# Kernel optimization log

Measured on AMD Instinct MI355X. Metric: run time of the kernel, lower is better.

The kernel has to match this reference:

```python
import jax, jax.numpy as jnp
import numpy as np

INF = 1e10
EPS = 1e-5
B, S, H, NH = 4, 1024, 1024, 16


def _linear(x, W, b):
    return x @ W + b


def _layernorm(x, g, b):
    mean = x.mean(-1, keepdims=True)
    var = ((x - mean) ** 2).mean(-1, keepdims=True)  # biased, matches .pow(2).mean
    return g * (x - mean) / jnp.sqrt(var + EPS) + b


def _mha(xq, xkv, mask, Wq, bq, Wk, bk, Wv, bv, Wo, bo, num_head):
    Bq, Sq, Hd = xq.shape
    d = Hd // num_head
    scale = jnp.asarray(np.sqrt(d), xq.dtype)
    q = _linear(xq, Wq, bq).reshape(Bq, Sq, num_head, d).transpose(0, 2, 1, 3)
    k = _linear(xkv, Wk, bk).reshape(Bq, -1, num_head, d).transpose(0, 2, 1, 3)
    v = _linear(xkv, Wv, bv).reshape(Bq, -1, num_head, d).transpose(0, 2, 1, 3)
    scores = jnp.einsum('bhqd,bhkd->bhqk', q, k) / scale
    # mask [B,Skv] -> additive; NOTE: original divides (scores+mask) by scale AGAIN
    add = (1.0 - mask[:, None, None, :].astype(scores.dtype)) * (-INF)
    att = jax.nn.softmax((scores + add) / scale, axis=-1)
    out = jnp.einsum('bhqk,bhkd->bhqd', att, v).transpose(0, 2, 1, 3).reshape(Bq, Sq, Hd)
    return _linear(out, Wo, bo)


def _block(hidden_states, self_att_mask, cross_hidden_states, cross_att_mask,
           sWq, sbq, sWk, sbk, sWv, sbv, sWo, sbo,
           cWq, cbq, cWk, cbk, cWv, cbv, cWo, cbo,
           g, b, W1, b1, W2, b2, num_head):
    sa = _mha(hidden_states, hidden_states, self_att_mask,
              sWq, sbq, sWk, sbk, sWv, sbv, sWo, sbo, num_head)
    sa_n = _layernorm(sa + hidden_states, g, b)
    ca = _mha(sa_n, cross_hidden_states, cross_att_mask,
              cWq, cbq, cWk, cbk, cWv, cbv, cWo, cbo, num_head)
    # NOTE: residual uses the ORIGINAL hidden_states, matching the source
    h = _layernorm(ca + hidden_states, g, b)
    ff = _linear(jax.nn.relu(_linear(h, W1, b1)), W2, b2)
    return _layernorm(ff + h, g, b)


def setup_inputs() -> dict:
    key = jax.random.key(0)
    ks = jax.random.split(key, 20)
    std = 0.02
    def lin(k, din, dout):
        k1, k2 = jax.random.split(k)
        return (jax.random.normal(k1, (din, dout), jnp.float32) * std,
                jax.random.normal(k2, (dout,), jnp.float32) * std)
    inp = {
        'hidden_states': jax.random.normal(ks[0], (B, S, H), jnp.float32),
        'self_att_mask': jnp.ones((B, S), jnp.int32),
        'cross_hidden_states': jax.random.normal(ks[1], (B, S, H), jnp.float32),
        'cross_att_mask': jnp.ones((B, S), jnp.int32),
        'num_head': NH,
    }
    names = ['sWq sbq', 'sWk sbk', 'sWv sbv', 'sWo sbo',
             'cWq cbq', 'cWk cbk', 'cWv cbv', 'cWo cbo']
    for i, nm in enumerate(names):
        wn, bn = nm.split()
        W, bb = lin(ks[2 + i], H, H)
        inp[wn] = W
        inp[bn] = bb
    inp['g'] = jnp.ones((H,), jnp.float32)
    inp['b'] = jnp.zeros((H,), jnp.float32)
    inp['W1'], inp['b1'] = lin(ks[12], H, 4 * H)
    inp['W2'], inp['b2'] = lin(ks[13], 4 * H, H)
    return inp


def reference(hidden_states, self_att_mask, cross_hidden_states, cross_att_mask,
              num_head, sWq, sbq, sWk, sbk, sWv, sbv, sWo, sbo,
              cWq, cbq, cWk, cbk, cWv, cbv, cWo, cbo,
              g, b, W1, b1, W2, b2):
    return _block(hidden_states, self_att_mask, cross_hidden_states, cross_att_mask,
                  sWq, sbq, sWk, sbk, sWv, sbv, sWo, sbo,
                  cWq, cbq, cWk, cbk, cWv, cbv, cWo, cbo,
                  g, b, W1, b1, W2, b2, num_head)
```

## Files before the change

kernel.cpp:

```cpp
#include <hip/hip_runtime.h>
#include <hip/hip_bf16.h>


typedef float float4v __attribute__((ext_vector_type(4)));
typedef __bf16 bf16x8 __attribute__((ext_vector_type(8)));
typedef unsigned short ushort8 __attribute__((ext_vector_type(8)));
typedef unsigned int uint2v __attribute__((ext_vector_type(2)));

__device__ __forceinline__ unsigned short f2bf1(float f) {
    unsigned u = __builtin_bit_cast(unsigned, f);
    u += 0x7fffu + ((u >> 16) & 1u);
    return (unsigned short)(u >> 16);
}
__device__ __forceinline__ unsigned f2bf2(float lo, float hi) {
    unsigned a = __builtin_bit_cast(unsigned, lo);
    a += 0x7fffu + ((a >> 16) & 1u);
    unsigned b = __builtin_bit_cast(unsigned, hi);
    b += 0x7fffu + ((b >> 16) & 1u);
    return (a >> 16) | (b & 0xffff0000u);
}
__device__ __forceinline__ bf16x8 ldsv8(const unsigned short* p) {
    return __builtin_bit_cast(bf16x8, *(const ushort8*)p);
}
__device__ __forceinline__ void async16(const unsigned short* g, unsigned short* l) {
    __builtin_amdgcn_global_load_lds(
        (const __attribute__((address_space(1))) unsigned int*)(g),
        (__attribute__((address_space(3))) unsigned int*)(l),
        16, 0, 0);
}

template <int RELU, int OUT_BF16, int DBUF, int ORDER>
__global__ __launch_bounds__(256) void gemm_bt(
    const unsigned short* __restrict__ A, const unsigned short* __restrict__ Bt,
    const float* __restrict__ bias, void* __restrict__ Cout,
    int M, int N, int K)
{
    __shared__ __align__(16) unsigned short As[(DBUF ? 2 : 1) * 128 * 64];
    __shared__ __align__(16) unsigned short Bs[(DBUF ? 2 : 1) * 128 * 64];

    const int tid = threadIdx.x;
    const int m0 = (ORDER ? blockIdx.x : blockIdx.y) * 128;
    const int n0 = (ORDER ? blockIdx.y : blockIdx.x) * 128;
    const int w = tid >> 6, lane = tid & 63;
    const int lr = lane & 15, quad = lane >> 4;
    const int wm = (w >> 1) * 64, wn = (w & 1) * 64;

    const int sr = lane >> 3, sc = lane & 7;
    const int fch = sc ^ sr;
    const unsigned short* Ag = A + (size_t)(m0 + w * 32 + sr) * K + fch * 8;
    const unsigned short* Bg = Bt + (size_t)(n0 + w * 32 + sr) * K + fch * 8;

    float4v acc[4][4];
#pragma unroll
    for (int i = 0; i < 4; i++)
#pragma unroll
        for (int j = 0; j < 4; j++) acc[i][j] = 0.f;

    const int ch0 = quad ^ (lr & 7);
    const int ch1 = (4 + quad) ^ (lr & 7);

    auto issue = [&](int buf, int k0) {
        unsigned short* Al = &As[buf * (128 * 64) + (w * 32) * 64];
        unsigned short* Bl = &Bs[buf * (128 * 64) + (w * 32) * 64];
#pragma unroll
        for (int i = 0; i < 4; i++) {
            async16(Ag + (size_t)(i * 8) * K + k0, Al + (i * 8) * 64);
            async16(Bg + (size_t)(i * 8) * K + k0, Bl + (i * 8) * 64);
        }
    };
    auto compute = [&](int buf) {
        const unsigned short* Ab = &As[buf * (128 * 64)];
        const unsigned short* Bb = &Bs[buf * (128 * 64)];
#pragma unroll
        for (int kk = 0; kk < 2; kk++) {
            const int ch = kk ? ch1 : ch0;
            bf16x8 af[4], bf[4];
#pragma unroll
            for (int i = 0; i < 4; i++) {
                af[i] = ldsv8(&Ab[(wm + i * 16 + lr) * 64 + ch * 8]);
                bf[i] = ldsv8(&Bb[(wn + i * 16 + lr) * 64 + ch * 8]);
            }
#pragma unroll
            for (int i = 0; i < 4; i++)
#pragma unroll
                for (int j = 0; j < 4; j++)
                    acc[i][j] = __builtin_amdgcn_mfma_f32_16x16x32_bf16(af[i], bf[j], acc[i][j], 0, 0, 0);
        }
    };

    if (DBUF) {
        const int NIT = K >> 6;
        issue(0, 0);
        for (int it = 0; it < NIT; ++it) {
            const int nxt = it + 1;
            if (nxt < NIT) {
                issue(nxt & 1, nxt << 6);
                __builtin_amdgcn_sched_barrier(0);
                __builtin_amdgcn_s_waitcnt(0x0F78);
            } else {
                __builtin_amdgcn_sched_barrier(0);
                __builtin_amdgcn_s_waitcnt(0x0F70);
            }
            __builtin_amdgcn_s_barrier();
            __builtin_amdgcn_sched_barrier(0);
            compute(it & 1);
            __builtin_amdgcn_sched_barrier(0);
            __builtin_amdgcn_s_barrier();
            __builtin_amdgcn_sched_barrier(0);
        }
    } else {
        for (int k0 = 0; k0 < K; k0 += 64) {
            issue(0, k0);
            __syncthreads();
            compute(0);
            __syncthreads();
        }
    }

#pragma unroll
    for (int j = 0; j < 4; j++) {
        const int col = n0 + wn + j * 16 + lr;
        const float bv = bias[col];
#pragma unroll
        for (int i = 0; i < 4; i++) {
            const int row0 = m0 + wm + i * 16 + quad * 4;
#pragma unroll
            for (int r = 0; r < 4; r++) {
                float v = acc[i][j][r] + bv;
                if (RELU) v = fmaxf(v, 0.f);
                if (OUT_BF16)
                    ((unsigned short*)Cout)[(size_t)(row0 + r) * N + col] = f2bf1(v);
                else
                    ((float*)Cout)[(size_t)(row0 + r) * N + col] = v;
            }
        }
    }
}

__global__ __launch_bounds__(256) void attn_mfma(
    const unsigned short* __restrict__ Q, int qs,
    const unsigned short* __restrict__ K, const unsigned short* __restrict__ V, int kvs,
    const int* __restrict__ mask, unsigned short* __restrict__ O)
{
    __shared__ __align__(16) unsigned short Ks[64 * 64];
    __shared__ __align__(16) unsigned short Vt[64][72];
    __shared__ __align__(16) unsigned short Pb[128][72];
    __shared__ float madd[64];

    const int tid = threadIdx.x;
    const int b = blockIdx.z, h = blockIdx.y, q0 = blockIdx.x * 128;
    const int w = tid >> 6, lane = tid & 63;
    const int lr = lane & 15, quad = lane >> 4;
    const int wm = w * 32;
    const float4v zf = {0.f, 0.f, 0.f, 0.f};

    bf16x8 qf[2][2];
#pragma unroll
    for (int i = 0; i < 2; i++)
#pragma unroll
        for (int c = 0; c < 2; c++)
            qf[i][c] = ldsv8(Q + (size_t)(b * 1024 + q0 + wm + i * 16 + lr) * qs
                             + h * 64 + c * 32 + quad * 8);

    const int sr = lane >> 3, sc = lane & 7;
    const int fch = sc ^ sr;
    const int ch0 = quad ^ (lr & 7), ch1 = (4 + quad) ^ (lr & 7);
    const int vkey = tid & 63, vseg = (tid >> 6) * 16;

    float4v oac[2][4];
    float m_reg[2][4], l_reg[2][4];
#pragma unroll
    for (int i = 0; i < 2; i++) {
#pragma unroll
        for (int j = 0; j < 4; j++) oac[i][j] = zf;
#pragma unroll
        for (int rr = 0; rr < 4; rr++) { m_reg[i][rr] = -3e38f; l_reg[i][rr] = 0.f; }
    }

    for (int kb = 0; kb < 16; ++kb) {
        const int s0 = kb * 64;
        __syncthreads();
#pragma unroll
        for (int i = 0; i < 2; i++)
            async16(K + (size_t)(b * 1024 + s0 + w * 16 + i * 8 + sr) * kvs + h * 64 + fch * 8,
                    &Ks[(w * 16 + i * 8) * 64]);
        {
            const unsigned short* vp = V + (size_t)(b * 1024 + s0 + vkey) * kvs + h * 64 + vseg;
            ushort8 v0 = *(const ushort8*)vp;
            ushort8 v1 = *(const ushort8*)(vp + 8);
#pragma unroll
            for (int j = 0; j < 8; j++) {
                Vt[vseg + j][vkey] = v0[j];
                Vt[vseg + 8 + j][vkey] = v1[j];
            }
        }
        if (tid < 64)
            madd[tid] = (1.0f - (float)mask[b * 1024 + s0 + tid]) * (-1.25e9f);
        __syncthreads();

        float4v sa[2][4];
#pragma unroll
        for (int j = 0; j < 4; j++) {
            const int krow = j * 16 + lr;
            bf16x8 kf0 = ldsv8(&Ks[krow * 64 + ch0 * 8]);
            bf16x8 kf1 = ldsv8(&Ks[krow * 64 + ch1 * 8]);
            sa[0][j] = __builtin_amdgcn_mfma_f32_16x16x32_bf16(qf[0][0], kf0, zf, 0, 0, 0);
            sa[0][j] = __builtin_amdgcn_mfma_f32_16x16x32_bf16(qf[0][1], kf1, sa[0][j], 0, 0, 0);
            sa[1][j] = __builtin_amdgcn_mfma_f32_16x16x32_bf16(qf[1][0], kf0, zf, 0, 0, 0);
            sa[1][j] = __builtin_amdgcn_mfma_f32_16x16x32_bf16(qf[1][1], kf1, sa[1][j], 0, 0, 0);
        }
#pragma unroll
        for (int j = 0; j < 4; j++) {
            const float ma = madd[j * 16 + lr];
            sa[0][j] = sa[0][j] * 0.015625f + ma;
            sa[1][j] = sa[1][j] * 0.015625f + ma;
        }

#pragma unroll
        for (int i = 0; i < 2; i++) {
#pragma unroll
            for (int rr = 0; rr < 4; rr++) {
                float rm = fmaxf(fmaxf(sa[i][0][rr], sa[i][1][rr]),
                                 fmaxf(sa[i][2][rr], sa[i][3][rr]));
                rm = fmaxf(rm, __shfl_xor(rm, 1));
                rm = fmaxf(rm, __shfl_xor(rm, 2));
                rm = fmaxf(rm, __shfl_xor(rm, 4));
                rm = fmaxf(rm, __shfl_xor(rm, 8));
                float mnew = fmaxf(m_reg[i][rr], rm);
                float al = __expf(m_reg[i][rr] - mnew);
                float p0 = __expf(sa[i][0][rr] - mnew);
                float p1 = __expf(sa[i][1][rr] - mnew);
                float p2 = __expf(sa[i][2][rr] - mnew);
                float p3 = __expf(sa[i][3][rr] - mnew);
                float rs = p0 + p1 + p2 + p3;
                rs += __shfl_xor(rs, 1);
                rs += __shfl_xor(rs, 2);
                rs += __shfl_xor(rs, 4);
                rs += __shfl_xor(rs, 8);
                l_reg[i][rr] = l_reg[i][rr] * al + rs;
                m_reg[i][rr] = mnew;
                const int row = wm + i * 16 + quad * 4 + rr;
                Pb[row][ 0 + lr] = f2bf1(p0);
                Pb[row][16 + lr] = f2bf1(p1);
                Pb[row][32 + lr] = f2bf1(p2);
                Pb[row][48 + lr] = f2bf1(p3);
                oac[i][0][rr] *= al;
                oac[i][1][rr] *= al;
                oac[i][2][rr] *= al;
                oac[i][3][rr] *= al;
            }
        }

        bf16x8 pf[2][2];
#pragma unroll
        for (int i = 0; i < 2; i++)
#pragma unroll
            for (int c = 0; c < 2; c++)
                pf[i][c] = ldsv8(&Pb[wm + i * 16 + lr][c * 32 + quad * 8]);
#pragma unroll
        for (int j = 0; j < 4; j++) {
            bf16x8 vf0 = ldsv8(&Vt[j * 16 + lr][quad * 8]);
            bf16x8 vf1 = ldsv8(&Vt[j * 16 + lr][32 + quad * 8]);
            oac[0][j] = __builtin_amdgcn_mfma_f32_16x16x32_bf16(pf[0][0], vf0, oac[0][j], 0, 0, 0);
            oac[0][j] = __builtin_amdgcn_mfma_f32_16x16x32_bf16(pf[0][1], vf1, oac[0][j], 0, 0, 0);
            oac[1][j] = __builtin_amdgcn_mfma_f32_16x16x32_bf16(pf[1][0], vf0, oac[1][j], 0, 0, 0);
            oac[1][j] = __builtin_amdgcn_mfma_f32_16x16x32_bf16(pf[1][1], vf1, oac[1][j], 0, 0, 0);
        }
    }

#pragma unroll
    for (int i = 0; i < 2; i++)
#pragma unroll
        for (int rr = 0; rr < 4; rr++) {
            const float inv = 1.0f / l_reg[i][rr];
            const int row = q0 + wm + i * 16 + quad * 4 + rr;
            unsigned short* op = O + (size_t)(b * 1024 + row) * 1024 + h * 64;
#pragma unroll
            for (int j = 0; j < 4; j++)
                op[j * 16 + lr] = f2bf1(oac[i][j][rr] * inv);
        }
}

__global__ __launch_bounds__(256) void add_ln_kernel(
    const float* __restrict__ X, const float* __restrict__ R,
    const float* __restrict__ g, const float* __restrict__ bb,
    float* __restrict__ outF, unsigned short* __restrict__ outB)
{
    const int row = blockIdx.x, tid = threadIdx.x;
    const float4v* x4 = (const float4v*)(X + (size_t)row * 1024);
    const float4v* r4 = (const float4v*)(R + (size_t)row * 1024);
    float4v z = x4[tid] + r4[tid];
    float s = z.x + z.y + z.z + z.w;
    float sq = z.x * z.x + z.y * z.y + z.z * z.z + z.w * z.w;
#pragma unroll
    for (int off = 32; off > 0; off >>= 1) {
        s += __shfl_down(s, off);
        sq += __shfl_down(sq, off);
    }
    __shared__ float ws[4], wsq[4];
    __shared__ float sm, sr;
    if ((tid & 63) == 0) { ws[tid >> 6] = s; wsq[tid >> 6] = sq; }
    __syncthreads();
    if (tid == 0) {
        float S1 = ws[0] + ws[1] + ws[2] + ws[3];
        float S2 = wsq[0] + wsq[1] + wsq[2] + wsq[3];
        float mean = S1 * (1.0f / 1024.0f);
        float var = S2 * (1.0f / 1024.0f) - mean * mean;
        sm = mean;
        sr = rsqrtf(var + 1e-5f);
    }
    __syncthreads();
    const float mean = sm, rstd = sr;
    const float4v* g4 = (const float4v*)g;
    const float4v* b4 = (const float4v*)bb;
    float4v res = g4[tid] * ((z - mean) * rstd) + b4[tid];
    if (outF) ((float4v*)(outF + (size_t)row * 1024))[tid] = res;
    if (outB) {
        uint2v u = { f2bf2(res.x, res.y), f2bf2(res.z, res.w) };
        *(uint2v*)(outB + (size_t)row * 1024 + tid * 4) = u;
    }
}

__device__ __forceinline__ void tconv_body(const float* __restrict__ S,
                                           unsigned short* __restrict__ D,
                                           int R, int C, int r0, int c0)
{
    __shared__ float tile[64][65];
    const int tid = threadIdx.x;
    const int tr = tid >> 4, tc4 = (tid & 15) * 4;
#pragma unroll
    for (int i = 0; i < 4; i++) {
        const int rr = i * 16 + tr;
        *(float4v*)&tile[rr][tc4] = *(const float4v*)(S + (size_t)(r0 + rr) * C + c0 + tc4);
    }
    __syncthreads();
#pragma unroll
    for (int i = 0; i < 4; i++) {
        const int dr = i * 16 + tr;
        float v0 = tile[tc4 + 0][dr];
        float v1 = tile[tc4 + 1][dr];
        float v2 = tile[tc4 + 2][dr];
        float v3 = tile[tc4 + 3][dr];
        uint2v u = { f2bf2(v0, v1), f2bf2(v2, v3) };
        *(uint2v*)(D + (size_t)(c0 + dr) * R + r0 + tc4) = u;
    }
}
__global__ __launch_bounds__(256) void transpose_conv(
    const float* __restrict__ S, unsigned short* __restrict__ D, int R, int C)
{
    tconv_body(S, D, R, C, blockIdx.y * 64, blockIdx.x * 64);
}
__global__ __launch_bounds__(256) void transpose8(
    const float* s0, const float* s1, const float* s2, const float* s3,
    const float* s4, const float* s5, const float* s6, const float* s7,
    unsigned short* d0, unsigned short* d1, unsigned short* d2, unsigned short* d3,
    unsigned short* d4, unsigned short* d5, unsigned short* d6, unsigned short* d7)
{
    const float* S;
    unsigned short* D;
    switch (blockIdx.z) {
        case 0: S = s0; D = d0; break;
        case 1: S = s1; D = d1; break;
        case 2: S = s2; D = d2; break;
        case 3: S = s3; D = d3; break;
        case 4: S = s4; D = d4; break;
        case 5: S = s5; D = d5; break;
        case 6: S = s6; D = d6; break;
        default: S = s7; D = d7; break;
    }
    tconv_body(S, D, 1024, 1024, blockIdx.y * 64, blockIdx.x * 64);
}

__global__ __launch_bounds__(256) void convert_bf16(
    const float* __restrict__ s0, unsigned short* __restrict__ d0,
    const float* __restrict__ s1, unsigned short* __restrict__ d1)
{
    const float* s = blockIdx.y ? s1 : s0;
    unsigned short* d = blockIdx.y ? d1 : d0;
    const size_t i = ((size_t)blockIdx.x * 256 + threadIdx.x) * 4;
    float4v v = *(const float4v*)(s + i);
    uint2v u = { f2bf2(v.x, v.y), f2bf2(v.z, v.w) };
    *(uint2v*)(d + i) = u;
}

__global__ __launch_bounds__(256) void biascat(
    const float* __restrict__ sbq, const float* __restrict__ sbk, const float* __restrict__ sbv,
    const float* __restrict__ cbk, const float* __restrict__ cbv,
    float* __restrict__ bq, float* __restrict__ bc)
{
    const int i = blockIdx.x * 256 + threadIdx.x;
    if (i < 3072)
        bq[i] = i < 1024 ? sbq[i] : (i < 2048 ? sbk[i - 1024] : sbv[i - 2048]);
    else {
        const int j = i - 3072;
        bc[j] = j < 1024 ? cbk[j] : cbv[j - 1024];
    }
}

extern "C" void kernel_launch(void* const* d_in, const int* in_sizes, int n_in,
                              void* d_out, int out_size, void* d_ws, size_t ws_size,
                              hipStream_t stream)
{
    const float* x     = (const float*)d_in[0];
    const int*   smask = (const int*)d_in[1];
    const float* cx    = (const float*)d_in[2];
    const int*   cmask = (const int*)d_in[3];
    const float* sWq = (const float*)d_in[5],  *sbq = (const float*)d_in[6];
    const float* sWk = (const float*)d_in[7],  *sbk = (const float*)d_in[8];
    const float* sWv = (const float*)d_in[9],  *sbv = (const float*)d_in[10];
    const float* sWo = (const float*)d_in[11], *sbo = (const float*)d_in[12];
    const float* cWq = (const float*)d_in[13], *cbq = (const float*)d_in[14];
    const float* cWk = (const float*)d_in[15], *cbk = (const float*)d_in[16];
    const float* cWv = (const float*)d_in[17], *cbv = (const float*)d_in[18];
    const float* cWo = (const float*)d_in[19], *cbo = (const float*)d_in[20];
    const float* g   = (const float*)d_in[21], *bb  = (const float*)d_in[22];
    const float* W1  = (const float*)d_in[23], *b1  = (const float*)d_in[24];
    const float* W2  = (const float*)d_in[25], *b2  = (const float*)d_in[26];
    float* out = (float*)d_out;

    const size_t MB = 1024 * 1024;
    unsigned char* ws = (unsigned char*)d_ws;
    unsigned short* xb   = (unsigned short*)(ws + 0 * MB);
    unsigned short* cxb  = (unsigned short*)(ws + 8 * MB);
    unsigned short* SANb = (unsigned short*)(ws + 16 * MB);
    unsigned short* QKV  = (unsigned short*)(ws + 24 * MB);
    unsigned short* CQ   = (unsigned short*)(ws + 24 * MB);
    unsigned short* CKV  = (unsigned short*)(ws + 32 * MB);
    unsigned short* T    = (unsigned short*)(ws + 48 * MB);
    float*          Af   = (float*)(ws + 56 * MB);
    float*          HH   = (float*)(ws + 72 * MB);
    unsigned short* HHb  = (unsigned short*)(ws + 88 * MB);
    unsigned short* WtQKV = (unsigned short*)(ws + 96 * MB);
    unsigned short* WtCKV = (unsigned short*)(ws + 102 * MB);
    unsigned short* WtSWO = (unsigned short*)(ws + 106 * MB);
    unsigned short* WtCWQ = (unsigned short*)(ws + 108 * MB);
    unsigned short* WtCWO = (unsigned short*)(ws + 110 * MB);
    unsigned short* WtW1  = (unsigned short*)(ws + 112 * MB);
    unsigned short* WtW2  = (unsigned short*)(ws + 120 * MB);
    float* biasQ = (float*)(ws + 128 * MB);
    float* biasC = (float*)(ws + 128 * MB + 16 * 1024);
    unsigned short* MID = (unsigned short*)(ws + 0 * MB);

    dim3 blk(256);

    convert_bf16<<<dim3(4096, 2), blk, 0, stream>>>(x, xb, cx, cxb);
    transpose8<<<dim3(16, 16, 8), blk, 0, stream>>>(
        sWq, sWk, sWv, cWk, cWv, sWo, cWq, cWo,
        WtQKV, WtQKV + 1024 * 1024, WtQKV + 2 * 1024 * 1024,
        WtCKV, WtCKV + 1024 * 1024,
        WtSWO, WtCWQ, WtCWO);
    transpose_conv<<<dim3(64, 16), blk, 0, stream>>>(W1, WtW1, 1024, 4096);
    transpose_conv<<<dim3(16, 64), blk, 0, stream>>>(W2, WtW2, 4096, 1024);
    biascat<<<20, blk, 0, stream>>>(sbq, sbk, sbv, cbk, cbv, biasQ, biasC);

    gemm_bt<0, 1, 0, 1><<<dim3(32, 24), blk, 0, stream>>>(xb, WtQKV, biasQ, QKV, 4096, 3072, 1024);
    attn_mfma<<<dim3(8, 16, 4), blk, 0, stream>>>(QKV, 3072, QKV + 1024, QKV + 2048, 3072, smask, T);
    gemm_bt<0, 0, 1, 1><<<dim3(32, 8), blk, 0, stream>>>(T, WtSWO, sbo, Af, 4096, 1024, 1024);
    add_ln_kernel<<<4096, blk, 0, stream>>>(Af, x, g, bb, nullptr, SANb);

    gemm_bt<0, 1, 1, 1><<<dim3(32, 8), blk, 0, stream>>>(SANb, WtCWQ, cbq, CQ, 4096, 1024, 1024);
    gemm_bt<0, 1, 1, 1><<<dim3(32, 16), blk, 0, stream>>>(cxb, WtCKV, biasC, CKV, 4096, 2048, 1024);
    attn_mfma<<<dim3(8, 16, 4), blk, 0, stream>>>(CQ, 1024, CKV, CKV + 1024, 2048, cmask, T);
    gemm_bt<0, 0, 1, 1><<<dim3(32, 8), blk, 0, stream>>>(T, WtCWO, cbo, Af, 4096, 1024, 1024);
    add_ln_kernel<<<4096, blk, 0, stream>>>(Af, x, g, bb, HH, HHb);

    gemm_bt<1, 1, 0, 0><<<dim3(32, 32), blk, 0, stream>>>(HHb, WtW1, b1, MID, 4096, 4096, 1024);
    gemm_bt<0, 0, 1, 1><<<dim3(32, 8), blk, 0, stream>>>(MID, WtW2, b2, Af, 4096, 1024, 4096);
    add_ln_kernel<<<4096, blk, 0, stream>>>(Af, HH, g, bb, out, nullptr);
}
```

Before: 582.3 us.

## Split-K the N=1024 GEMMs and shrink attention tiles with swizzled LDS

```diff
diff --git a/kernel.cpp b/kernel.cpp
--- a/kernel.cpp
+++ b/kernel.cpp
@@ -41,14 +41,16 @@
     const int tid = threadIdx.x;
     const int m0 = (ORDER ? blockIdx.x : blockIdx.y) * 128;
     const int n0 = (ORDER ? blockIdx.y : blockIdx.x) * 128;
+    const int KL = K / gridDim.z;
+    const int kbase = blockIdx.z * KL;
     const int w = tid >> 6, lane = tid & 63;
     const int lr = lane & 15, quad = lane >> 4;
     const int wm = (w >> 1) * 64, wn = (w & 1) * 64;
 
     const int sr = lane >> 3, sc = lane & 7;
     const int fch = sc ^ sr;
-    const unsigned short* Ag = A + (size_t)(m0 + w * 32 + sr) * K + fch * 8;
-    const unsigned short* Bg = Bt + (size_t)(n0 + w * 32 + sr) * K + fch * 8;
+    const unsigned short* Ag = A + (size_t)(m0 + w * 32 + sr) * K + kbase + fch * 8;
+    const unsigned short* Bg = Bt + (size_t)(n0 + w * 32 + sr) * K + kbase + fch * 8;
 
     float4v acc[4][4];
 #pragma unroll
@@ -89,7 +91,7 @@
     };
 
     if (DBUF) {
-        const int NIT = K >> 6;
+        const int NIT = KL >> 6;
         issue(0, 0);
         for (int it = 0; it < NIT; ++it) {
             const int nxt = it + 1;
@@ -109,7 +111,7 @@
             __builtin_amdgcn_sched_barrier(0);
         }
     } else {
-        for (int k0 = 0; k0 < K; k0 += 64) {
+        for (int k0 = 0; k0 < KL; k0 += 64) {
             issue(0, k0);
             __syncthreads();
             compute(0);
@@ -120,7 +122,7 @@
 #pragma unroll
     for (int j = 0; j < 4; j++) {
         const int col = n0 + wn + j * 16 + lr;
-        const float bv = bias[col];
+        const float bv = bias ? bias[col] : 0.f;
 #pragma unroll
         for (int i = 0; i < 4; i++) {
             const int row0 = m0 + wm + i * 16 + quad * 4;
@@ -131,7 +133,7 @@
                 if (OUT_BF16)
                     ((unsigned short*)Cout)[(size_t)(row0 + r) * N + col] = f2bf1(v);
                 else
-                    ((float*)Cout)[(size_t)(row0 + r) * N + col] = v;
+                    ((float*)Cout)[(size_t)blockIdx.z * M * N + (size_t)(row0 + r) * N + col] = v;
             }
         }
     }
@@ -143,39 +145,38 @@
     const int* __restrict__ mask, unsigned short* __restrict__ O)
 {
     __shared__ __align__(16) unsigned short Ks[64 * 64];
-    __shared__ __align__(16) unsigned short Vt[64][72];
-    __shared__ __align__(16) unsigned short Pb[128][72];
+    __shared__ __align__(16) unsigned short Vt[64 * 64];
+    __shared__ __align__(16) unsigned short Pb[64 * 64];
     __shared__ float madd[64];
 
     const int tid = threadIdx.x;
-    const int b = blockIdx.z, h = blockIdx.y, q0 = blockIdx.x * 128;
+    const int b = blockIdx.z, h = blockIdx.y, q0 = blockIdx.x * 64;
     const int w = tid >> 6, lane = tid & 63;
     const int lr = lane & 15, quad = lane >> 4;
-    const int wm = w * 32;
     const float4v zf = {0.f, 0.f, 0.f, 0.f};
 
-    bf16x8 qf[2][2];
-#pragma unroll
-    for (int i = 0; i < 2; i++)
-#pragma unroll
-        for (int c = 0; c < 2; c++)
-            qf[i][c] = ldsv8(Q + (size_t)(b * 1024 + q0 + wm + i * 16 + lr) * qs
-                             + h * 64 + c * 32 + quad * 8);
+    bf16x8 qf[2];
+#pragma unroll
+    for (int c = 0; c < 2; c++)
+        qf[c] = ldsv8(Q + (size_t)(b * 1024 + q0 + w * 16 + lr) * qs
+                      + h * 64 + c * 32 + quad * 8);
 
     const int sr = lane >> 3, sc = lane & 7;
     const int fch = sc ^ sr;
     const int ch0 = quad ^ (lr & 7), ch1 = (4 + quad) ^ (lr & 7);
-    const int vkey = tid & 63, vseg = (tid >> 6) * 16;
-
-    float4v oac[2][4];
-    float m_reg[2][4], l_reg[2][4];
-#pragma unroll
-    for (int i = 0; i < 2; i++) {
-#pragma unroll
-        for (int j = 0; j < 4; j++) oac[i][j] = zf;
-#pragma unroll
-        for (int rr = 0; rr < 4; rr++) { m_reg[i][rr] = -3e38f; l_reg[i][rr] = 0.f; }
-    }
+
+    const int vk = tid & 15, vh = tid >> 7;
+    const int vkb = vk + vh * 32;
+    const int vseg = ((tid >> 4) & 7) * 8;
+    const int pospair = vk * 4 + vh * 2;
+    const int vchunk = pospair >> 3, voff = pospair & 7;
+
+    float4v oac[4];
+    float m_reg[4], l_reg[4];
+#pragma unroll
+    for (int j = 0; j < 4; j++) oac[j] = zf;
+#pragma unroll
+    for (int rr = 0; rr < 4; rr++) { m_reg[rr] = -3e38f; l_reg[rr] = 0.f; }
 
     for (int kb = 0; kb < 16; ++kb) {
         const int s0 = kb * 64;
@@ -185,111 +186,98 @@
             async16(K + (size_t)(b * 1024 + s0 + w * 16 + i * 8 + sr) * kvs + h * 64 + fch * 8,
                     &Ks[(w * 16 + i * 8) * 64]);
         {
-            const unsigned short* vp = V + (size_t)(b * 1024 + s0 + vkey) * kvs + h * 64 + vseg;
+            const unsigned short* vp = V + (size_t)(b * 1024 + s0 + vkb) * kvs + h * 64 + vseg;
             ushort8 v0 = *(const ushort8*)vp;
-            ushort8 v1 = *(const ushort8*)(vp + 8);
+            ushort8 v1 = *(const ushort8*)(vp + (size_t)16 * kvs);
 #pragma unroll
             for (int j = 0; j < 8; j++) {
-                Vt[vseg + j][vkey] = v0[j];
-                Vt[vseg + 8 + j][vkey] = v1[j];
+                const int row = vseg + j;
+                const int schv = vchunk ^ (row & 7);
+                *(unsigned*)&Vt[row * 64 + schv * 8 + voff] =
+                    (unsigned)v0[j] | ((unsigned)v1[j] << 16);
             }
         }
         if (tid < 64)
             madd[tid] = (1.0f - (float)mask[b * 1024 + s0 + tid]) * (-1.25e9f);
         __syncthreads();
 
-        float4v sa[2][4];
+        float4v sa[4];
 #pragma unroll
         for (int j = 0; j < 4; j++) {
             const int krow = j * 16 + lr;
             bf16x8 kf0 = ldsv8(&Ks[krow * 64 + ch0 * 8]);
             bf16x8 kf1 = ldsv8(&Ks[krow * 64 + ch1 * 8]);
-            sa[0][j] = __builtin_amdgcn_mfma_f32_16x16x32_bf16(qf[0][0], kf0, zf, 0, 0, 0);
-            sa[0][j] = __builtin_amdgcn_mfma_f32_16x16x32_bf16(qf[0][1], kf1, sa[0][j], 0, 0, 0);
-            sa[1][j] = __builtin_amdgcn_mfma_f32_16x16x32_bf16(qf[1][0], kf0, zf, 0, 0, 0);
-            sa[1][j] = __builtin_amdgcn_mfma_f32_16x16x32_bf16(qf[1][1], kf1, sa[1][j], 0, 0, 0);
-        }
+            sa[j] = __builtin_amdgcn_mfma_f32_16x16x32_bf16(qf[0], kf0, zf, 0, 0, 0);
+            sa[j] = __builtin_amdgcn_mfma_f32_16x16x32_bf16(qf[1], kf1, sa[j], 0, 0, 0);
+        }
+#pragma unroll
+        for (int j = 0; j < 4; j++)
+            sa[j] = sa[j] * 0.015625f + madd[j * 16 + lr];
+
+#pragma unroll
+        for (int rr = 0; rr < 4; rr++) {
+            float rm = fmaxf(fmaxf(sa[0][rr], sa[1][rr]), fmaxf(sa[2][rr], sa[3][rr]));
+            rm = fmaxf(rm, __shfl_xor(rm, 1));
+            rm = fmaxf(rm, __shfl_xor(rm, 2));
+            rm = fmaxf(rm, __shfl_xor(rm, 4));
+            rm = fmaxf(rm, __shfl_xor(rm, 8));
+            const float mnew = fmaxf(m_reg[rr], rm);
+            const float al = __expf(m_reg[rr] - mnew);
+            const float p0 = __expf(sa[0][rr] - mnew);
+            const float p1 = __expf(sa[1][rr] - mnew);
+            const float p2 = __expf(sa[2][rr] - mnew);
+            const float p3 = __expf(sa[3][rr] - mnew);
+            float rs = p0 + p1 + p2 + p3;
+            rs += __shfl_xor(rs, 1);
+            rs += __shfl_xor(rs, 2);
+            rs += __shfl_xor(rs, 4);
+            rs += __shfl_xor(rs, 8);
+            l_reg[rr] = l_reg[rr] * al + rs;
+            m_reg[rr] = mnew;
+            const int row = w * 16 + quad * 4 + rr;
+            const int schp = (lr >> 1) ^ (row & 7);
+            uint2v pk = { f2bf2(p0, p1), f2bf2(p2, p3) };
+            *(uint2v*)&Pb[row * 64 + schp * 8 + (lr & 1) * 4] = pk;
+            oac[0][rr] *= al;
+            oac[1][rr] *= al;
+            oac[2][rr] *= al;
+            oac[3][rr] *= al;
+        }
+
+        bf16x8 pf0 = ldsv8(&Pb[(w * 16 + lr) * 64 + ch0 * 8]);
+        bf16x8 pf1 = ldsv8(&Pb[(w * 16 + lr) * 64 + ch1 * 8]);
 #pragma unroll
         for (int j = 0; j < 4; j++) {
-            const float ma = madd[j * 16 + lr];
-            sa[0][j] = sa[0][j] * 0.015625f + ma;
-            sa[1][j] = sa[1][j] * 0.015625f + ma;
-        }
-
-#pragma unroll
-        for (int i = 0; i < 2; i++) {
-#pragma unroll
-            for (int rr = 0; rr < 4; rr++) {
-                float rm = fmaxf(fmaxf(sa[i][0][rr], sa[i][1][rr]),
-                                 fmaxf(sa[i][2][rr], sa[i][3][rr]));
-                rm = fmaxf(rm, __shfl_xor(rm, 1));
-                rm = fmaxf(rm, __shfl_xor(rm, 2));
-                rm = fmaxf(rm, __shfl_xor(rm, 4));
-                rm = fmaxf(rm, __shfl_xor(rm, 8));
-                float mnew = fmaxf(m_reg[i][rr], rm);
-                float al = __expf(m_reg[i][rr] - mnew);
-                float p0 = __expf(sa[i][0][rr] - mnew);
-                float p1 = __expf(sa[i][1][rr] - mnew);
-                float p2 = __expf(sa[i][2][rr] - mnew);
-                float p3 = __expf(sa[i][3][rr] - mnew);
-                float rs = p0 + p1 + p2 + p3;
-                rs += __shfl_xor(rs, 1);
-                rs += __shfl_xor(rs, 2);
-                rs += __shfl_xor(rs, 4);
-                rs += __shfl_xor(rs, 8);
-                l_reg[i][rr] = l_reg[i][rr] * al + rs;
-                m_reg[i][rr] = mnew;
-                const int row = wm + i * 16 + quad * 4 + rr;
-                Pb[row][ 0 + lr] = f2bf1(p0);
-                Pb[row][16 + lr] = f2bf1(p1);
-                Pb[row][32 + lr] = f2bf1(p2);
-                Pb[row][48 + lr] = f2bf1(p3);
-                oac[i][0][rr] *= al;
-                oac[i][1][rr] *= al;
-                oac[i][2][rr] *= al;
-                oac[i][3][rr] *= al;
-            }
-        }
-
-        bf16x8 pf[2][2];
-#pragma unroll
-        for (int i = 0; i < 2; i++)
-#pragma unroll
-            for (int c = 0; c < 2; c++)
-                pf[i][c] = ldsv8(&Pb[wm + i * 16 + lr][c * 32 + quad * 8]);
-#pragma unroll
-        for (int j = 0; j < 4; j++) {
-            bf16x8 vf0 = ldsv8(&Vt[j * 16 + lr][quad * 8]);
-            bf16x8 vf1 = ldsv8(&Vt[j * 16 + lr][32 + quad * 8]);
-            oac[0][j] = __builtin_amdgcn_mfma_f32_16x16x32_bf16(pf[0][0], vf0, oac[0][j], 0, 0, 0);
-            oac[0][j] = __builtin_amdgcn_mfma_f32_16x16x32_bf16(pf[0][1], vf1, oac[0][j], 0, 0, 0);
-            oac[1][j] = __builtin_amdgcn_mfma_f32_16x16x32_bf16(pf[1][0], vf0, oac[1][j], 0, 0, 0);
-            oac[1][j] = __builtin_amdgcn_mfma_f32_16x16x32_bf16(pf[1][1], vf1, oac[1][j], 0, 0, 0);
-        }
-    }
-
-#pragma unroll
-    for (int i = 0; i < 2; i++)
-#pragma unroll
-        for (int rr = 0; rr < 4; rr++) {
-            const float inv = 1.0f / l_reg[i][rr];
-            const int row = q0 + wm + i * 16 + quad * 4 + rr;
-            unsigned short* op = O + (size_t)(b * 1024 + row) * 1024 + h * 64;
-#pragma unroll
-            for (int j = 0; j < 4; j++)
-                op[j * 16 + lr] = f2bf1(oac[i][j][rr] * inv);
-        }
-}
-
+            bf16x8 vf0 = ldsv8(&Vt[(j * 16 + lr) * 64 + ch0 * 8]);
+            bf16x8 vf1 = ldsv8(&Vt[(j * 16 + lr) * 64 + ch1 * 8]);
+            oac[j] = __builtin_amdgcn_mfma_f32_16x16x32_bf16(pf0, vf0, oac[j], 0, 0, 0);
+            oac[j] = __builtin_amdgcn_mfma_f32_16x16x32_bf16(pf1, vf1, oac[j], 0, 0, 0);
+        }
+    }
+
+#pragma unroll
+    for (int rr = 0; rr < 4; rr++) {
+        const float inv = 1.0f / l_reg[rr];
+        const int row = q0 + w * 16 + quad * 4 + rr;
+        unsigned short* op = O + (size_t)(b * 1024 + row) * 1024 + h * 64;
+#pragma unroll
+        for (int j = 0; j < 4; j++)
+            op[j * 16 + lr] = f2bf1(oac[j][rr] * inv);
+    }
+}
+
+#define PSTRIDE ((size_t)4096 * 1024)
 __global__ __launch_bounds__(256) void add_ln_kernel(
-    const float* __restrict__ X, const float* __restrict__ R,
+    const float* __restrict__ P, int nparts, const float* __restrict__ lbias,
+    const float* __restrict__ R,
     const float* __restrict__ g, const float* __restrict__ bb,
     float* __restrict__ outF, unsigned short* __restrict__ outB)
 {
     const int row = blockIdx.x, tid = threadIdx.x;
-    const float4v* x4 = (const float4v*)(X + (size_t)row * 1024);
-    const float4v* r4 = (const float4v*)(R + (size_t)row * 1024);
-    float4v z = x4[tid] + r4[tid];
+    float4v z = ((const float4v*)(R + (size_t)row * 1024))[tid];
+    for (int p = 0; p < nparts; ++p)
+        z += ((const float4v*)(P + p * PSTRIDE + (size_t)row * 1024))[tid];
+    if (lbias) z += ((const float4v*)lbias)[tid];
     float s = z.x + z.y + z.z + z.w;
     float sq = z.x * z.x + z.y * z.y + z.z * z.z + z.w * z.w;
 #pragma unroll
@@ -423,23 +411,23 @@
     unsigned short* xb   = (unsigned short*)(ws + 0 * MB);
     unsigned short* cxb  = (unsigned short*)(ws + 8 * MB);
     unsigned short* SANb = (unsigned short*)(ws + 16 * MB);
-    unsigned short* QKV  = (unsigned short*)(ws + 24 * MB);
     unsigned short* CQ   = (unsigned short*)(ws + 24 * MB);
+    unsigned short* MID  = (unsigned short*)(ws + 0 * MB);
+    unsigned short* QKV  = (unsigned short*)(ws + 32 * MB);
     unsigned short* CKV  = (unsigned short*)(ws + 32 * MB);
-    unsigned short* T    = (unsigned short*)(ws + 48 * MB);
-    float*          Af   = (float*)(ws + 56 * MB);
-    float*          HH   = (float*)(ws + 72 * MB);
-    unsigned short* HHb  = (unsigned short*)(ws + 88 * MB);
-    unsigned short* WtQKV = (unsigned short*)(ws + 96 * MB);
-    unsigned short* WtCKV = (unsigned short*)(ws + 102 * MB);
-    unsigned short* WtSWO = (unsigned short*)(ws + 106 * MB);
-    unsigned short* WtCWQ = (unsigned short*)(ws + 108 * MB);
-    unsigned short* WtCWO = (unsigned short*)(ws + 110 * MB);
-    unsigned short* WtW1  = (unsigned short*)(ws + 112 * MB);
-    unsigned short* WtW2  = (unsigned short*)(ws + 120 * MB);
-    float* biasQ = (float*)(ws + 128 * MB);
-    float* biasC = (float*)(ws + 128 * MB + 16 * 1024);
-    unsigned short* MID = (unsigned short*)(ws + 0 * MB);
+    unsigned short* T    = (unsigned short*)(ws + 56 * MB);
+    float*          P    = (float*)(ws + 64 * MB);
+    float*          HH   = (float*)(ws + 96 * MB);
+    unsigned short* HHb  = (unsigned short*)(ws + 112 * MB);
+    unsigned short* WtQKV = (unsigned short*)(ws + 120 * MB);
+    unsigned short* WtCKV = (unsigned short*)(ws + 126 * MB);
+    unsigned short* WtSWO = (unsigned short*)(ws + 130 * MB);
+    unsigned short* WtCWQ = (unsigned short*)(ws + 132 * MB);
+    unsigned short* WtCWO = (unsigned short*)(ws + 134 * MB);
+    unsigned short* WtW1  = (unsigned short*)(ws + 136 * MB);
+    unsigned short* WtW2  = (unsigned short*)(ws + 144 * MB);
+    float* biasQ = (float*)(ws + 152 * MB);
+    float* biasC = (float*)(ws + 152 * MB + 16 * 1024);
 
     dim3 blk(256);
 
@@ -454,17 +442,17 @@
     biascat<<<20, blk, 0, stream>>>(sbq, sbk, sbv, cbk, cbv, biasQ, biasC);
 
     gemm_bt<0, 1, 0, 1><<<dim3(32, 24), blk, 0, stream>>>(xb, WtQKV, biasQ, QKV, 4096, 3072, 1024);
-    attn_mfma<<<dim3(8, 16, 4), blk, 0, stream>>>(QKV, 3072, QKV + 1024, QKV + 2048, 3072, smask, T);
-    gemm_bt<0, 0, 1, 1><<<dim3(32, 8), blk, 0, stream>>>(T, WtSWO, sbo, Af, 4096, 1024, 1024);
-    add_ln_kernel<<<4096, blk, 0, stream>>>(Af, x, g, bb, nullptr, SANb);
+    attn_mfma<<<dim3(16, 16, 4), blk, 0, stream>>>(QKV, 3072, QKV + 1024, QKV + 2048, 3072, smask, T);
+    gemm_bt<0, 0, 1, 1><<<dim3(32, 8, 2), blk, 0, stream>>>(T, WtSWO, nullptr, P, 4096, 1024, 1024);
+    add_ln_kernel<<<4096, blk, 0, stream>>>(P, 2, sbo, x, g, bb, nullptr, SANb);
 
     gemm_bt<0, 1, 1, 1><<<dim3(32, 8), blk, 0, stream>>>(SANb, WtCWQ, cbq, CQ, 4096, 1024, 1024);
     gemm_bt<0, 1, 1, 1><<<dim3(32, 16), blk, 0, stream>>>(cxb, WtCKV, biasC, CKV, 4096, 2048, 1024);
-    attn_mfma<<<dim3(8, 16, 4), blk, 0, stream>>>(CQ, 1024, CKV, CKV + 1024, 2048, cmask, T);
-    gemm_bt<0, 0, 1, 1><<<dim3(32, 8), blk, 0, stream>>>(T, WtCWO, cbo, Af, 4096, 1024, 1024);
-    add_ln_kernel<<<4096, blk, 0, stream>>>(Af, x, g, bb, HH, HHb);
+    attn_mfma<<<dim3(16, 16, 4), blk, 0, stream>>>(CQ, 1024, CKV, CKV + 1024, 2048, cmask, T);
+    gemm_bt<0, 0, 1, 1><<<dim3(32, 8, 2), blk, 0, stream>>>(T, WtCWO, nullptr, P, 4096, 1024, 1024);
+    add_ln_kernel<<<4096, blk, 0, stream>>>(P, 2, cbo, x, g, bb, HH, HHb);
 
     gemm_bt<1, 1, 0, 0><<<dim3(32, 32), blk, 0, stream>>>(HHb, WtW1, b1, MID, 4096, 4096, 1024);
-    gemm_bt<0, 0, 1, 1><<<dim3(32, 8), blk, 0, stream>>>(MID, WtW2, b2, Af, 4096, 1024, 4096);
-    add_ln_kernel<<<4096, blk, 0, stream>>>(Af, HH, g, bb, out, nullptr);
-}
+    gemm_bt<0, 0, 1, 1><<<dim3(32, 8, 2), blk, 0, stream>>>(MID, WtW2, nullptr, P, 4096, 1024, 4096);
+    add_ln_kernel<<<4096, blk, 0, stream>>>(P, 2, b2, HH, g, bb, out, nullptr);
+}
```

Measured after the change: 528.5 us. 9.2% less time.

## Split-K output GEMMs, pre-transpose V in epilogue, drop online softmax max

Applied to the files above, without the earlier changes.

```diff
diff --git a/kernel.cpp b/kernel.cpp
--- a/kernel.cpp
+++ b/kernel.cpp
@@ -6,6 +6,8 @@
 typedef __bf16 bf16x8 __attribute__((ext_vector_type(8)));
 typedef unsigned short ushort8 __attribute__((ext_vector_type(8)));
 typedef unsigned int uint2v __attribute__((ext_vector_type(2)));
+
+#define VBIG (1 << 29)
 
 __device__ __forceinline__ unsigned short f2bf1(float f) {
     unsigned u = __builtin_bit_cast(unsigned, f);
@@ -33,7 +35,8 @@
 __global__ __launch_bounds__(256) void gemm_bt(
     const unsigned short* __restrict__ A, const unsigned short* __restrict__ Bt,
     const float* __restrict__ bias, void* __restrict__ Cout,
-    int M, int N, int K)
+    int M, int N, int K, int ldc, int qcols, int vcol0,
+    unsigned short* __restrict__ VTout)
 {
     __shared__ __align__(16) unsigned short As[(DBUF ? 2 : 1) * 128 * 64];
     __shared__ __align__(16) unsigned short Bs[(DBUF ? 2 : 1) * 128 * 64];
@@ -41,14 +44,16 @@
     const int tid = threadIdx.x;
     const int m0 = (ORDER ? blockIdx.x : blockIdx.y) * 128;
     const int n0 = (ORDER ? blockIdx.y : blockIdx.x) * 128;
+    const int KL = K / gridDim.z;
+    const int kbase = blockIdx.z * KL;
     const int w = tid >> 6, lane = tid & 63;
     const int lr = lane & 15, quad = lane >> 4;
     const int wm = (w >> 1) * 64, wn = (w & 1) * 64;
 
     const int sr = lane >> 3, sc = lane & 7;
     const int fch = sc ^ sr;
-    const unsigned short* Ag = A + (size_t)(m0 + w * 32 + sr) * K + fch * 8;
-    const unsigned short* Bg = Bt + (size_t)(n0 + w * 32 + sr) * K + fch * 8;
+    const unsigned short* Ag = A + (size_t)(m0 + w * 32 + sr) * K + kbase + fch * 8;
+    const unsigned short* Bg = Bt + (size_t)(n0 + w * 32 + sr) * K + kbase + fch * 8;
 
     float4v acc[4][4];
 #pragma unroll
@@ -89,7 +94,7 @@
     };
 
     if (DBUF) {
-        const int NIT = K >> 6;
+        const int NIT = KL >> 6;
         issue(0, 0);
         for (int it = 0; it < NIT; ++it) {
             const int nxt = it + 1;
@@ -109,7 +114,7 @@
             __builtin_amdgcn_sched_barrier(0);
         }
     } else {
-        for (int k0 = 0; k0 < K; k0 += 64) {
+        for (int k0 = 0; k0 < KL; k0 += 64) {
             issue(0, k0);
             __syncthreads();
             compute(0);
@@ -117,21 +122,42 @@
         }
     }
 
+    if (n0 >= vcol0) {
+        const int crel = n0 - vcol0 + wn;
+        const int hh = crel >> 6;
+        const int bidx = (m0 + wm) >> 10;
+        const int tbase = ((m0 + wm) & 1023) + quad * 16;
+#pragma unroll
+        for (int j = 0; j < 4; j++) {
+            const float bv = bias ? bias[n0 + wn + j * 16 + lr] : 0.f;
+            const int d = j * 16 + lr;
+            unsigned short* vp = VTout + ((size_t)(bidx * 16 + hh) * 64 + d) * 1024 + tbase;
+#pragma unroll
+            for (int r = 0; r < 4; r++) {
+                uint2v u = { f2bf2(acc[0][j][r] + bv, acc[1][j][r] + bv),
+                             f2bf2(acc[2][j][r] + bv, acc[3][j][r] + bv) };
+                *(uint2v*)(vp + r * 4) = u;
+            }
+        }
+        return;
+    }
+
+    const float qs = (n0 < qcols) ? 0.015625f : 1.0f;
 #pragma unroll
     for (int j = 0; j < 4; j++) {
         const int col = n0 + wn + j * 16 + lr;
-        const float bv = bias[col];
+        const float bv = bias ? bias[col] : 0.f;
 #pragma unroll
         for (int i = 0; i < 4; i++) {
             const int row0 = m0 + wm + i * 16 + quad * 4;
 #pragma unroll
             for (int r = 0; r < 4; r++) {
-                float v = acc[i][j][r] + bv;
+                float v = (acc[i][j][r] + bv) * qs;
                 if (RELU) v = fmaxf(v, 0.f);
                 if (OUT_BF16)
-                    ((unsigned short*)Cout)[(size_t)(row0 + r) * N + col] = f2bf1(v);
+                    ((unsigned short*)Cout)[(size_t)(row0 + r) * ldc + col] = f2bf1(v);
                 else
-                    ((float*)Cout)[(size_t)(row0 + r) * N + col] = v;
+                    ((float*)Cout)[(size_t)blockIdx.z * M * ldc + (size_t)(row0 + r) * ldc + col] = v;
             }
         }
     }
@@ -139,13 +165,14 @@
 
 __global__ __launch_bounds__(256) void attn_mfma(
     const unsigned short* __restrict__ Q, int qs,
-    const unsigned short* __restrict__ K, const unsigned short* __restrict__ V, int kvs,
-    const int* __restrict__ mask, unsigned short* __restrict__ O)
+    const unsigned short* __restrict__ K, int kvs,
+    const unsigned short* __restrict__ VT,
+    const float* __restrict__ maskf,
+    unsigned short* __restrict__ O)
 {
     __shared__ __align__(16) unsigned short Ks[64 * 64];
-    __shared__ __align__(16) unsigned short Vt[64][72];
-    __shared__ __align__(16) unsigned short Pb[128][72];
-    __shared__ float madd[64];
+    __shared__ __align__(16) unsigned short Vt[64 * 64];
+    __shared__ __align__(16) unsigned short Pb[128 * 64];
 
     const int tid = threadIdx.x;
     const int b = blockIdx.z, h = blockIdx.y, q0 = blockIdx.x * 128;
@@ -165,37 +192,32 @@
     const int sr = lane >> 3, sc = lane & 7;
     const int fch = sc ^ sr;
     const int ch0 = quad ^ (lr & 7), ch1 = (4 + quad) ^ (lr & 7);
-    const int vkey = tid & 63, vseg = (tid >> 6) * 16;
+    const unsigned short* VTb = VT + (size_t)(b * 16 + h) * 64 * 1024;
 
     float4v oac[2][4];
-    float m_reg[2][4], l_reg[2][4];
+    float lsum[2][4];
 #pragma unroll
     for (int i = 0; i < 2; i++) {
 #pragma unroll
         for (int j = 0; j < 4; j++) oac[i][j] = zf;
 #pragma unroll
-        for (int rr = 0; rr < 4; rr++) { m_reg[i][rr] = -3e38f; l_reg[i][rr] = 0.f; }
+        for (int rr = 0; rr < 4; rr++) lsum[i][rr] = 0.f;
     }
 
     for (int kb = 0; kb < 16; ++kb) {
         const int s0 = kb * 64;
         __syncthreads();
 #pragma unroll
-        for (int i = 0; i < 2; i++)
+        for (int i = 0; i < 2; i++) {
             async16(K + (size_t)(b * 1024 + s0 + w * 16 + i * 8 + sr) * kvs + h * 64 + fch * 8,
                     &Ks[(w * 16 + i * 8) * 64]);
-        {
-            const unsigned short* vp = V + (size_t)(b * 1024 + s0 + vkey) * kvs + h * 64 + vseg;
-            ushort8 v0 = *(const ushort8*)vp;
-            ushort8 v1 = *(const ushort8*)(vp + 8);
-#pragma unroll
-            for (int j = 0; j < 8; j++) {
-                Vt[vseg + j][vkey] = v0[j];
-                Vt[vseg + 8 + j][vkey] = v1[j];
-            }
-        }
-        if (tid < 64)
-            madd[tid] = (1.0f - (float)mask[b * 1024 + s0 + tid]) * (-1.25e9f);
+            async16(VTb + (size_t)(w * 16 + i * 8 + sr) * 1024 + s0 + fch * 8,
+                    &Vt[(w * 16 + i * 8) * 64]);
+        }
+        float mf[4];
+#pragma unroll
+        for (int j = 0; j < 4; j++)
+            mf[j] = maskf[b * 1024 + s0 + j * 16 + lr];
         __syncthreads();
 
         float4v sa[2][4];
@@ -209,58 +231,33 @@
             sa[1][j] = __builtin_amdgcn_mfma_f32_16x16x32_bf16(qf[1][0], kf0, zf, 0, 0, 0);
             sa[1][j] = __builtin_amdgcn_mfma_f32_16x16x32_bf16(qf[1][1], kf1, sa[1][j], 0, 0, 0);
         }
+
+#pragma unroll
+        for (int i = 0; i < 2; i++) {
+#pragma unroll
+            for (int rr = 0; rr < 4; rr++) {
+                const float p0 = __expf(sa[i][0][rr]) * mf[0];
+                const float p1 = __expf(sa[i][1][rr]) * mf[1];
+                const float p2 = __expf(sa[i][2][rr]) * mf[2];
+                const float p3 = __expf(sa[i][3][rr]) * mf[3];
+                lsum[i][rr] += (p0 + p1) + (p2 + p3);
+                const int row = wm + i * 16 + quad * 4 + rr;
+                const int schp = (lr >> 1) ^ (row & 7);
+                uint2v pk = { f2bf2(p0, p1), f2bf2(p2, p3) };
+                *(uint2v*)&Pb[row * 64 + schp * 8 + (lr & 1) * 4] = pk;
+            }
+        }
+
+        bf16x8 pf[2][2];
+#pragma unroll
+        for (int i = 0; i < 2; i++)
+#pragma unroll
+            for (int c = 0; c < 2; c++)
+                pf[i][c] = ldsv8(&Pb[(wm + i * 16 + lr) * 64 + (c ? ch1 : ch0) * 8]);
 #pragma unroll
         for (int j = 0; j < 4; j++) {
-            const float ma = madd[j * 16 + lr];
-            sa[0][j] = sa[0][j] * 0.015625f + ma;
-            sa[1][j] = sa[1][j] * 0.015625f + ma;
-        }
-
-#pragma unroll
-        for (int i = 0; i < 2; i++) {
-#pragma unroll
-            for (int rr = 0; rr < 4; rr++) {
-                float rm = fmaxf(fmaxf(sa[i][0][rr], sa[i][1][rr]),
-                                 fmaxf(sa[i][2][rr], sa[i][3][rr]));
-                rm = fmaxf(rm, __shfl_xor(rm, 1));
-                rm = fmaxf(rm, __shfl_xor(rm, 2));
-                rm = fmaxf(rm, __shfl_xor(rm, 4));
-                rm = fmaxf(rm, __shfl_xor(rm, 8));
-                float mnew = fmaxf(m_reg[i][rr], rm);
-                float al = __expf(m_reg[i][rr] - mnew);
-                float p0 = __expf(sa[i][0][rr] - mnew);
-                float p1 = __expf(sa[i][1][rr] - mnew);
-                float p2 = __expf(sa[i][2][rr] - mnew);
-                float p3 = __expf(sa[i][3][rr] - mnew);
-                float rs = p0 + p1 + p2 + p3;
-                rs += __shfl_xor(rs, 1);
-                rs += __shfl_xor(rs, 2);
-                rs += __shfl_xor(rs, 4);
-                rs += __shfl_xor(rs, 8);
-                l_reg[i][rr] = l_reg[i][rr] * al + rs;
-                m_reg[i][rr] = mnew;
-                const int row = wm + i * 16 + quad * 4 + rr;
-                Pb[row][ 0 + lr] = f2bf1(p0);
-                Pb[row][16 + lr] = f2bf1(p1);
-                Pb[row][32 + lr] = f2bf1(p2);
-                Pb[row][48 + lr] = f2bf1(p3);
-                oac[i][0][rr] *= al;
-                oac[i][1][rr] *= al;
-                oac[i][2][rr] *= al;
-                oac[i][3][rr] *= al;
-            }
-        }
-
-        bf16x8 pf[2][2];
-#pragma unroll
-        for (int i = 0; i < 2; i++)
-#pragma unroll
-            for (int c = 0; c < 2; c++)
-                pf[i][c] = ldsv8(&Pb[wm + i * 16 + lr][c * 32 + quad * 8]);
-#pragma unroll
-        for (int j = 0; j < 4; j++) {
-            bf16x8 vf0 = ldsv8(&Vt[j * 16 + lr][quad * 8]);
-            bf16x8 vf1 = ldsv8(&Vt[j * 16 + lr][32 + quad * 8]);
+            bf16x8 vf0 = ldsv8(&Vt[(j * 16 + lr) * 64 + ch0 * 8]);
+            bf16x8 vf1 = ldsv8(&Vt[(j * 16 + lr) * 64 + ch1 * 8]);
             oac[0][j] = __builtin_amdgcn_mfma_f32_16x16x32_bf16(pf[0][0], vf0, oac[0][j], 0, 0, 0);
             oac[0][j] = __builtin_amdgcn_mfma_f32_16x16x32_bf16(pf[0][1], vf1, oac[0][j], 0, 0, 0);
             oac[1][j] = __builtin_amdgcn_mfma_f32_16x16x32_bf16(pf[1][0], vf0, oac[1][j], 0, 0, 0);
@@ -272,7 +269,12 @@
     for (int i = 0; i < 2; i++)
 #pragma unroll
         for (int rr = 0; rr < 4; rr++) {
-            const float inv = 1.0f / l_reg[i][rr];
+            float l = lsum[i][rr];
+            l += __shfl_xor(l, 1);
+            l += __shfl_xor(l, 2);
+            l += __shfl_xor(l, 4);
+            l += __shfl_xor(l, 8);
+            const float inv = 1.0f / l;
             const int row = q0 + wm + i * 16 + quad * 4 + rr;
             unsigned short* op = O + (size_t)(b * 1024 + row) * 1024 + h * 64;
 #pragma unroll
@@ -281,15 +283,18 @@
         }
 }
 
+#define PSTRIDE ((size_t)4096 * 1024)
 __global__ __launch_bounds__(256) void add_ln_kernel(
-    const float* __restrict__ X, const float* __restrict__ R,
+    const float* __restrict__ P, int nparts, const float* __restrict__ lbias,
+    const float* __restrict__ R,
     const float* __restrict__ g, const float* __restrict__ bb,
     float* __restrict__ outF, unsigned short* __restrict__ outB)
 {
     const int row = blockIdx.x, tid = threadIdx.x;
-    const float4v* x4 = (const float4v*)(X + (size_t)row * 1024);
-    const float4v* r4 = (const float4v*)(R + (size_t)row * 1024);
-    float4v z = x4[tid] + r4[tid];
+    float4v z = ((const float4v*)(R + (size_t)row * 1024))[tid];
+    for (int p = 0; p < nparts; ++p)
+        z += ((const float4v*)(P + p * PSTRIDE + (size_t)row * 1024))[tid];
+    if (lbias) z += ((const float4v*)lbias)[tid];
     float s = z.x + z.y + z.z + z.w;
     float sq = z.x * z.x + z.y * z.y + z.z * z.z + z.w * z.w;
 #pragma unroll
@@ -386,15 +391,20 @@
 __global__ __launch_bounds__(256) void biascat(
     const float* __restrict__ sbq, const float* __restrict__ sbk, const float* __restrict__ sbv,
     const float* __restrict__ cbk, const float* __restrict__ cbv,
-    float* __restrict__ bq, float* __restrict__ bc)
+    const int* __restrict__ smask, const int* __restrict__ cmask,
+    float* __restrict__ bq, float* __restrict__ bc,
+    float* __restrict__ smf, float* __restrict__ cmf)
 {
     const int i = blockIdx.x * 256 + threadIdx.x;
     if (i < 3072)
         bq[i] = i < 1024 ? sbq[i] : (i < 2048 ? sbk[i - 1024] : sbv[i - 2048]);
-    else {
+    else if (i < 5120) {
         const int j = i - 3072;
         bc[j] = j < 1024 ? cbk[j] : cbv[j - 1024];
-    }
+    } else if (i < 9216)
+        smf[i - 5120] = (float)smask[i - 5120];
+    else
+        cmf[i - 9216] = (float)cmask[i - 9216];
 }
 
 extern "C" void kernel_launch(void* const* d_in, const int* in_sizes, int n_in,
@@ -423,23 +433,27 @@
     unsigned short* xb   = (unsigned short*)(ws + 0 * MB);
     unsigned short* cxb  = (unsigned short*)(ws + 8 * MB);
     unsigned short* SANb = (unsigned short*)(ws + 16 * MB);
-    unsigned short* QKV  = (unsigned short*)(ws + 24 * MB);
     unsigned short* CQ   = (unsigned short*)(ws + 24 * MB);
-    unsigned short* CKV  = (unsigned short*)(ws + 32 * MB);
-    unsigned short* T    = (unsigned short*)(ws + 48 * MB);
-    float*          Af   = (float*)(ws + 56 * MB);
-    float*          HH   = (float*)(ws + 72 * MB);
-    unsigned short* HHb  = (unsigned short*)(ws + 88 * MB);
-    unsigned short* WtQKV = (unsigned short*)(ws + 96 * MB);
-    unsigned short* WtCKV = (unsigned short*)(ws + 102 * MB);
-    unsigned short* WtSWO = (unsigned short*)(ws + 106 * MB);
-    unsigned short* WtCWQ = (unsigned short*)(ws + 108 * MB);
-    unsigned short* WtCWO = (unsigned short*)(ws + 110 * MB);
-    unsigned short* WtW1  = (unsigned short*)(ws + 112 * MB);
-    unsigned short* WtW2  = (unsigned short*)(ws + 120 * MB);
-    float* biasQ = (float*)(ws + 128 * MB);
-    float* biasC = (float*)(ws + 128 * MB + 16 * 1024);
-    unsigned short* MID = (unsigned short*)(ws + 0 * MB);
+    unsigned short* MID  = (unsigned short*)(ws + 0 * MB);
+    unsigned short* QK   = (unsigned short*)(ws + 32 * MB);
+    unsigned short* VTs  = (unsigned short*)(ws + 48 * MB);
+    float*          P    = (float*)(ws + 32 * MB);
+    unsigned short* CKb  = (unsigned short*)(ws + 56 * MB);
+    unsigned short* VTc  = (unsigned short*)(ws + 64 * MB);
+    unsigned short* T    = (unsigned short*)(ws + 72 * MB);
+    float*          HH   = (float*)(ws + 80 * MB);
+    unsigned short* HHb  = (unsigned short*)(ws + 96 * MB);
+    unsigned short* WtQKV = (unsigned short*)(ws + 104 * MB);
+    unsigned short* WtCKV = (unsigned short*)(ws + 110 * MB);
+    unsigned short* WtSWO = (unsigned short*)(ws + 114 * MB);
+    unsigned short* WtCWQ = (unsigned short*)(ws + 116 * MB);
+    unsigned short* WtCWO = (unsigned short*)(ws + 118 * MB);
+    unsigned short* WtW1  = (unsigned short*)(ws + 120 * MB);
+    unsigned short* WtW2  = (unsigned short*)(ws + 128 * MB);
+    float* biasQ = (float*)(ws + 136 * MB);
+    float* biasC = (float*)(ws + 136 * MB + 16 * 1024);
+    float* smf   = (float*)(ws + 136 * MB + 32 * 1024);
+    float* cmf   = (float*)(ws + 136 * MB + 48 * 1024);
 
     dim3 blk(256);
 
@@ -451,20 +465,28 @@
         WtSWO, WtCWQ, WtCWO);
     transpose_conv<<<dim3(64, 16), blk, 0, stream>>>(W1, WtW1, 1024, 4096);
     transpose_conv<<<dim3(16, 64), blk, 0, stream>>>(W2, WtW2, 4096, 1024);
-    biascat<<<20, blk, 0, stream>>>(sbq, sbk, sbv, cbk, cbv, biasQ, biasC);
-
-    gemm_bt<0, 1, 0, 1><<<dim3(32, 24), blk, 0, stream>>>(xb, WtQKV, biasQ, QKV, 4096, 3072, 1024);
-    attn_mfma<<<dim3(8, 16, 4), blk, 0, stream>>>(QKV, 3072, QKV + 1024, QKV + 2048, 3072, smask, T);
-    gemm_bt<0, 0, 1, 1><<<dim3(32, 8), blk, 0, stream>>>(T, WtSWO, sbo, Af, 4096, 1024, 1024);
-    add_ln_kernel<<<4096, blk, 0, stream>>>(Af, x, g, bb, nullptr, SANb);
-
-    gemm_bt<0, 1, 1, 1><<<dim3(32, 8), blk, 0, stream>>>(SANb, WtCWQ, cbq, CQ, 4096, 1024, 1024);
-    gemm_bt<0, 1, 1, 1><<<dim3(32, 16), blk, 0, stream>>>(cxb, WtCKV, biasC, CKV, 4096, 2048, 1024);
-    attn_mfma<<<dim3(8, 16, 4), blk, 0, stream>>>(CQ, 1024, CKV, CKV + 1024, 2048, cmask, T);
-    gemm_bt<0, 0, 1, 1><<<dim3(32, 8), blk, 0, stream>>>(T, WtCWO, cbo, Af, 4096, 1024, 1024);
-    add_ln_kernel<<<4096, blk, 0, stream>>>(Af, x, g, bb, HH, HHb);
-
-    gemm_bt<1, 1, 0, 0><<<dim3(32, 32), blk, 0, stream>>>(HHb, WtW1, b1, MID, 4096, 4096, 1024);
-    gemm_bt<0, 0, 1, 1><<<dim3(32, 8), blk, 0, stream>>>(MID, WtW2, b2, Af, 4096, 1024, 4096);
-    add_ln_kernel<<<4096, blk, 0, stream>>>(Af, HH, g, bb, out, nullptr);
-}
+    biascat<<<52, blk, 0, stream>>>(sbq, sbk, sbv, cbk, cbv, smask, cmask,
+                                    biasQ, biasC, smf, cmf);
+
+    gemm_bt<0, 1, 0, 1><<<dim3(32, 24), blk, 0, stream>>>(
+        xb, WtQKV, biasQ, QK, 4096, 3072, 1024, 2048, 1024, 2048, VTs);
+    attn_mfma<<<dim3(8, 16, 4), blk, 0, stream>>>(QK, 2048, QK + 1024, 2048, VTs, smf, T);
+    gemm_bt<0, 0, 1, 1><<<dim3(32, 8, 2), blk, 0, stream>>>(
+        T, WtSWO, nullptr, P, 4096, 1024, 1024, 1024, 0, VBIG, nullptr);
+    add_ln_kernel<<<4096, blk, 0, stream>>>(P, 2, sbo, x, g, bb, nullptr, SANb);
+
+    gemm_bt<0, 1, 1, 1><<<dim3(32, 8), blk, 0, stream>>>(
+        SANb, WtCWQ, cbq, CQ, 4096, 1024, 1024, 1024, 1024, VBIG, nullptr);
+    gemm_bt<0, 1, 1, 1><<<dim3(32, 16), blk, 0, stream>>>(
+        cxb, WtCKV, biasC, CKb, 4096, 2048, 1024, 1024, 0, 1024, VTc);
+    attn_mfma<<<dim3(8, 16, 4), blk, 0, stream>>>(CQ, 1024, CKb, 1024, VTc, cmf, T);
+    gemm_bt<0, 0, 1, 1><<<dim3(32, 8, 2), blk, 0, stream>>>(
+        T, WtCWO, nullptr, P, 4096, 1024, 1024, 1024, 0, VBIG, nullptr);
+    add_ln_kernel<<<4096, blk, 0, stream>>>(P, 2, cbo, x, g, bb, HH, HHb);
+
+    gemm_bt<1, 1, 0, 0><<<dim3(32, 32), blk, 0, stream>>>(
+        HHb, WtW1, b1, MID, 4096, 4096, 1024, 4096, 0, VBIG, nullptr);
+    gemm_bt<0, 0, 1, 1><<<dim3(32, 8, 2), blk, 0, stream>>>(
+        MID, WtW2, nullptr, P, 4096, 1024, 4096, 1024, 0, VBIG, nullptr);
+    add_ln_kernel<<<4096, blk, 0, stream>>>(P, 2, b2, HH, g, bb, out, nullptr);
+}
```

New measurement: 490.2 us. 15.8% less time.
